# Performance work log

Measured on AMD Instinct MI355X. Metric: run time of the kernel, lower is better.

Reference implementation:

```python
import jax, jax.numpy as jnp
import numpy as np
import math

B, LQ, S, D = 8, 4096, 77, 1024
H, HD = 16, 64
R, ALPHA = 192, 16.0
LORA_SCALE = ALPHA / R
N_SUBJ = 32


def setup_inputs() -> dict:
    key = jax.random.key(0)
    ks = jax.random.split(key, 16)
    w = 0.02
    return {
        "hidden_states": jax.random.normal(ks[0], (B, LQ, D), jnp.float32),
        "encoder_hidden_states": jax.random.normal(ks[1], (B, S, D), jnp.float32),
        "Wq": jax.random.normal(ks[2], (D, D), jnp.float32) * w,
        "Wk": jax.random.normal(ks[3], (D, D), jnp.float32) * w,
        "Wv": jax.random.normal(ks[4], (D, D), jnp.float32) * w,
        "Wo": jax.random.normal(ks[5], (D, D), jnp.float32) * w,
        "bo": jnp.zeros((D,), jnp.float32),
        "Ak": jax.random.normal(ks[6], (R, D), jnp.float32) * w,
        "Bk": jax.random.normal(ks[7], (D, R), jnp.float32) * w,
        "Av": jax.random.normal(ks[8], (R, D), jnp.float32) * w,
        "Bv": jax.random.normal(ks[9], (D, R), jnp.float32) * w,
        "Ao": jax.random.normal(ks[10], (R, D), jnp.float32) * w,
        "Bo": jax.random.normal(ks[11], (D, R), jnp.float32) * w,
        "cross_attn_scale_factor": jnp.ones((), jnp.float32),
        "subj_b": jax.random.randint(ks[12], (N_SUBJ,), 0, B, jnp.int32),
        "subj_n": jax.random.randint(ks[13], (N_SUBJ,), 0, S, jnp.int32),
    }


def _lora(x, A, Bm):
    # peft LoRA delta: scale * (x @ A^T) @ B^T
    return LORA_SCALE * ((x @ A.T) @ Bm.T)


def reference(hidden_states, encoder_hidden_states, Wq, Wk, Wv, Wo, bo,
              Ak, Bk, Av, Bv, Ao, Bo, cross_attn_scale_factor, subj_b, subj_n):
    hs, ehs = hidden_states, encoder_hidden_states
    # q_lora_updates_query=False -> query uses the base projection only
    q = hs @ Wq.T                                  # [B, LQ, D]
    k = ehs @ Wk.T + _lora(ehs, Ak, Bk)            # [B, S, D] (to_k_lora)
    v = ehs @ Wv.T + _lora(ehs, Av, Bv)            # [B, S, D] (to_v_lora)

    q = q.reshape(B, LQ, H, HD).transpose(0, 2, 1, 3)   # [B,H,LQ,HD]
    k = k.reshape(B, S, H, HD).transpose(0, 2, 1, 3)    # [B,H,S,HD]
    v = v.reshape(B, S, H, HD).transpose(0, 2, 1, 3)

    scale = 1.0 / math.sqrt(HD)
    attn_score = jnp.einsum('bhld,bhsd->bhls', q, k) * scale  # [B,H,LQ,S]

    # normalize_cross_attn: zero-center subject-token scores over query dim,
    # then rescale by the learned cross_attn_scale_factor.
    sub = attn_score[subj_b, :, :, subj_n]                    # [K,H,LQ]
    sub = (sub - sub.mean(axis=2, keepdims=True)) * cross_attn_scale_factor
    attn_score = attn_score.at[subj_b, :, :, subj_n].set(sub)

    attn_weight = jax.nn.softmax(attn_score, axis=-1)
    out = jnp.einsum('bhls,bhsd->bhld', attn_weight, v)       # [B,H,LQ,HD]
    out = out.transpose(0, 2, 1, 3).reshape(B, LQ, D)

    # to_out_lora: base out-proj (with bias) + LoRA delta; to_out[1] dropout = id
    out = out @ Wo.T + bo + _lora(out, Ao, Bo)
    return out
```

## Files before the change

kernel.cpp:

```cpp
#include <hip/hip_runtime.h>
#include <stdint.h>

#define B_     8
#define LQ_    4096
#define S_     77
#define SP_    80
#define D_     1024
#define H_     16
#define HD_    64
#define NC_    1280
#define NSUBJ_ 32

typedef __attribute__((ext_vector_type(4))) float  f4;
typedef __attribute__((ext_vector_type(8))) short  short8;
typedef __attribute__((ext_vector_type(8))) unsigned short us8;
typedef __attribute__((ext_vector_type(4))) unsigned short us4;

__device__ __forceinline__ unsigned short f2bf(float f) {
  union { float f; unsigned u; } x; x.f = f;
  unsigned r = x.u + 0x7FFFu + ((x.u >> 16) & 1u);
  return (unsigned short)(r >> 16);
}

__device__ __forceinline__ void gload16(const void* g, void* s) {
  __builtin_amdgcn_global_load_lds((const __attribute__((address_space(1))) void*)g,
                                   (__attribute__((address_space(3))) void*)s, 16, 0, 0);
}

__global__ __launch_bounds__(256) void k_hssum(const float* __restrict__ hs,
                                               float* __restrict__ part,
                                               unsigned short* __restrict__ hsb) {
  int b = blockIdx.y;
  size_t base = ((size_t)b * LQ_ + (size_t)blockIdx.x * 64) * D_ + threadIdx.x * 4;
  f4 acc = {0.f, 0.f, 0.f, 0.f};
  for (int l = 0; l < 64; ++l) {
    f4 v = *(const f4*)(hs + base + (size_t)l * D_);
    acc += v;
    if (hsb) {
      us4 o;
#pragma unroll
      for (int j = 0; j < 4; ++j) o[j] = f2bf(v[j]);
      *(us4*)(hsb + base + (size_t)l * D_) = o;
    }
  }
  *(f4*)(part + (size_t)blockIdx.x * (B_ * D_) + b * D_ + threadIdx.x * 4) = acc;
}

__global__ __launch_bounds__(256) void k_hsred(const float* __restrict__ part,
                                               float* __restrict__ hssum) {
  int i = blockIdx.x * 256 + threadIdx.x;
  float s = 0.f;
  for (int x = 0; x < 64; ++x) s += part[(size_t)x * (B_ * D_) + i];
  hssum[i] = s;
}

__global__ __launch_bounds__(256) void k_tr4(const float* __restrict__ Wq, const float* __restrict__ Ak,
                                             const float* __restrict__ Av, const float* __restrict__ Ao,
                                             float* __restrict__ wqT, float* __restrict__ akT,
                                             float* __restrict__ avT, float* __restrict__ aoT) {
  int z = blockIdx.z;
  const float* in = z == 0 ? Wq : (z == 1 ? Ak : (z == 2 ? Av : Ao));
  float* out = z == 0 ? wqT : (z == 1 ? akT : (z == 2 ? avT : aoT));
  int R = z == 0 ? 1024 : 192;
  const int C = 1024;
  int c0 = blockIdx.x * 32, r0 = blockIdx.y * 32;
  if (r0 >= R) return;
  __shared__ float tile[32][33];
  int tx = threadIdx.x & 31, ty = threadIdx.x >> 5;
#pragma unroll
  for (int k = 0; k < 4; ++k)
    tile[ty + 8 * k][tx] = in[(size_t)(r0 + ty + 8 * k) * C + c0 + tx];
  __syncthreads();
#pragma unroll
  for (int k = 0; k < 4; ++k)
    out[(size_t)(c0 + ty + 8 * k) * R + r0 + tx] = tile[tx][ty + 8 * k];
}

template <bool OBF>
__device__ __forceinline__ void gemm64_body(
    const float* __restrict__ A, int lda, const float* __restrict__ Bt, int ldb,
    void* __restrict__ Cv, int ldc, long cbase, const float* __restrict__ Dm, int ldd,
    int M, int Mv, int N, int K, float alpha, int m0, int n0,
    short* As, short* Bs) {
  int t = threadIdx.x, lane = t & 63, wid = t >> 6;
  int wm = wid >> 1, wn = wid & 1;
  f4 acc[2][2] = {};
  int srow = t >> 2, skc = (t & 3) * 8;
  for (int k0 = 0; k0 < K; k0 += 32) {
    __syncthreads();
    f4 a0 = {0,0,0,0}, a1 = {0,0,0,0}, b0 = {0,0,0,0}, b1 = {0,0,0,0};
    if (m0 + srow < Mv) {
      const float* p = A + (size_t)(m0 + srow) * lda + k0 + skc;
      a0 = *(const f4*)p; a1 = *(const f4*)(p + 4);
    }
    if (n0 + srow < N) {
      const float* p = Bt + (size_t)(n0 + srow) * ldb + k0 + skc;
      b0 = *(const f4*)p; b1 = *(const f4*)(p + 4);
    }
    us8 ua, ub;
#pragma unroll
    for (int j = 0; j < 4; ++j) {
      ua[j] = f2bf(a0[j]); ua[4 + j] = f2bf(a1[j]);
      ub[j] = f2bf(b0[j]); ub[4 + j] = f2bf(b1[j]);
    }
    *(us8*)(As + srow * 40 + skc) = ua;
    *(us8*)(Bs + srow * 40 + skc) = ub;
    __syncthreads();
    short8 fa[2], fb[2];
#pragma unroll
    for (int i = 0; i < 2; ++i) {
      fa[i] = *(const short8*)(As + (wm * 32 + i * 16 + (lane & 15)) * 40 + (lane >> 4) * 8);
      fb[i] = *(const short8*)(Bs + (wn * 32 + i * 16 + (lane & 15)) * 40 + (lane >> 4) * 8);
    }
#pragma unroll
    for (int mi = 0; mi < 2; ++mi)
#pragma unroll
      for (int ni = 0; ni < 2; ++ni)
        acc[mi][ni] = __builtin_amdgcn_mfma_f32_16x16x32_bf16(fa[mi], fb[ni], acc[mi][ni], 0, 0, 0);
  }
#pragma unroll
  for (int mi = 0; mi < 2; ++mi)
#pragma unroll
    for (int ni = 0; ni < 2; ++ni)
#pragma unroll
      for (int j = 0; j < 4; ++j) {
        int row = m0 + wm * 32 + mi * 16 + (lane >> 4) * 4 + j;
        int col = n0 + wn * 32 + ni * 16 + (lane & 15);
        if (row < M && col < N) {
          float val = acc[mi][ni][j] * alpha;
          if (Dm) val += Dm[(size_t)row * ldd + col];
          size_t idx = (size_t)cbase + (size_t)row * ldc + col;
          if (OBF) ((unsigned short*)Cv)[idx] = f2bf(val);
          else     ((float*)Cv)[idx] = val;
        }
      }
}

template <bool OBF>
__global__ __launch_bounds__(256) void k_gemm_small(
    const float* __restrict__ A, int lda, long sA1, long sA2,
    const float* __restrict__ Bt, int ldb, long sB1, long sB2,
    void* __restrict__ Cv, int ldc, long sC1, long sC2,
    const float* __restrict__ Dm, int ldd,
    int M, int Mv, int N, int K, float alpha, int Z2) {
  int z = blockIdx.z, z1 = z / Z2, z2 = z - z1 * Z2;
  __shared__ short As[64 * 40];
  __shared__ short Bs[64 * 40];
  gemm64_body<OBF>(A + z1 * sA1 + z2 * sA2, lda, Bt + z1 * sB1 + z2 * sB2, ldb,
                   Cv, ldc, z1 * sC1 + z2 * sC2, Dm, ldd, M, Mv, N, K, alpha,
                   blockIdx.x * 64, blockIdx.y * 64, As, Bs);
}

__global__ __launch_bounds__(256) void k_weff(
    const float* __restrict__ Bk, const float* __restrict__ Bv, const float* __restrict__ Bo,
    const float* __restrict__ akT, const float* __restrict__ avT, const float* __restrict__ aoT,
    const float* __restrict__ Wk, const float* __restrict__ Wv, const float* __restrict__ Wo,
    float* __restrict__ weff, float alpha) {
  int z = blockIdx.z;
  const float* A  = z == 0 ? Bk : (z == 1 ? Bv : Bo);
  const float* Bt = z == 0 ? akT : (z == 1 ? avT : aoT);
  const float* Dm = z == 0 ? Wk : (z == 1 ? Wv : Wo);
  __shared__ short As[64 * 40];
  __shared__ short Bs[64 * 40];
  gemm64_body<false>(A, 192, Bt, 192, weff + (size_t)z * 1048576, 1024, 0, Dm, 1024,
                     1024, 1024, 1024, 192, alpha, blockIdx.x * 64, blockIdx.y * 64, As, Bs);
}

__global__ void k_mubeta(const float* __restrict__ hssum, const float* __restrict__ Wq,
                         const float* __restrict__ kv,
                         const int* __restrict__ sb, const int* __restrict__ sn,
                         const float* __restrict__ csf_p,
                         float* __restrict__ alphav, float* __restrict__ betav) {
  int h = blockIdx.x, b = blockIdx.y;
  int t = threadIdx.x;
  __shared__ float qp[64];
  {
    int hd = t >> 1, half = t & 1;
    const float* wr = Wq + (size_t)(h * 64 + hd) * D_ + half * 512;
    const float* hp = hssum + b * D_ + half * 512;
    float s = 0.f;
    for (int d = 0; d < 512; d += 4) {
      f4 w = *(const f4*)(wr + d);
      f4 x = *(const f4*)(hp + d);
      s += w[0] * x[0] + w[1] * x[1] + w[2] * x[2] + w[3] * x[3];
    }
    s += __shfl_xor(s, 1, 64);
    if (half == 0) qp[hd] = s * (1.f / 4096.f);
  }
  __syncthreads();
  int s = t;
  if (s >= SP_) return;
  const float* kp = kv + ((size_t)(b * SP_ + s)) * 2048 + h * HD_;
  float mu = 0.f;
#pragma unroll 8
  for (int hd = 0; hd < HD_; ++hd) mu += qp[hd] * kp[hd];
  mu *= 0.125f;
  bool subj = false;
  for (int i = 0; i < NSUBJ_; ++i) subj = subj || (sb[i] == b && sn[i] == s);
  float csf = *csf_p;
  int c = b * NC_ + h * SP_ + s;
  alphav[c] = subj ? csf : 1.f;
  betav[c] = (s >= S_) ? -1e30f : (subj ? -mu * csf : 0.f);
}

__global__ __launch_bounds__(512, 2) void k_score_big(
    const unsigned short* __restrict__ hsb, const unsigned short* __restrict__ Mt,
    const float* __restrict__ alphav, const float* __restrict__ betav,
    unsigned short* __restrict__ P) {
  extern __shared__ short lds[];
  const int ASZ = 256 * 64;
  const int BSZ = 320 * 64;
  int id = blockIdx.x;
  int x = id & 7, idp = id >> 3;
  int nt = idp & 3;
  int pid = (idp >> 2) * 8 + x;
  int b = pid >> 4, mt = pid & 15;
  int m0 = mt * 256, n0 = nt * 320;

  const unsigned short* Ab = hsb + (size_t)b * LQ_ * D_;
  const unsigned short* Bb = Mt + (size_t)b * NC_ * D_;
  const float* alp = alphav + b * NC_;
  const float* bet = betav + b * NC_;
  unsigned short* Pb = P + (size_t)b * LQ_ * NC_;

  int t = threadIdx.x, lane = t & 63, wid = t >> 6;
  int wm = wid >> 2, wn = wid & 3;
  f4 acc[8][5] = {};

  auto STAGE = [&](int bf, int k0) {
#pragma unroll
    for (int p = 0; p < 4; ++p) {
      int cb = p * 512 + wid * 64;
      int c = cb + lane;
      int row = c >> 3, col = ((c & 7) ^ (row & 7)) * 8;
      gload16(Ab + (size_t)(m0 + row) * D_ + k0 + col, (char*)(lds + bf * ASZ) + cb * 16);
    }
#pragma unroll
    for (int p = 0; p < 5; ++p) {
      int cb = p * 512 + wid * 64;
      int c = cb + lane;
      int row = c >> 3, col = ((c & 7) ^ (row & 7)) * 8;
      gload16(Bb + (size_t)(n0 + row) * D_ + k0 + col, (char*)(lds + 2 * ASZ + bf * BSZ) + cb * 16);
    }
  };

  STAGE(0, 0);
  int c = 0;
  for (int kt = 0; kt < 16; ++kt) {
    if (kt < 15) {
      STAGE(c ^ 1, (kt + 1) * 64);
      asm volatile("s_waitcnt vmcnt(9)" ::: "memory");
    } else {
      asm volatile("s_waitcnt vmcnt(0)" ::: "memory");
    }
    __builtin_amdgcn_s_barrier();
    const short* Ar = lds + c * ASZ;
    const short* Br = lds + 2 * ASZ + c * BSZ;
    __builtin_amdgcn_s_setprio(1);
#pragma unroll
    for (int kk = 0; kk < 2; ++kk) {
      int co = ((kk * 4 + (lane >> 4)) ^ (lane & 7)) * 8;
      short8 fb[5];
#pragma unroll
      for (int ni = 0; ni < 5; ++ni)
        fb[ni] = *(const short8*)(Br + (wn * 80 + ni * 16 + (lane & 15)) * 64 + co);
#pragma unroll
      for (int mi = 0; mi < 8; ++mi) {
        short8 fa = *(const short8*)(Ar + (wm * 128 + mi * 16 + (lane & 15)) * 64 + co);
#pragma unroll
        for (int ni = 0; ni < 5; ++ni)
          acc[mi][ni] = __builtin_amdgcn_mfma_f32_16x16x32_bf16(fa, fb[ni], acc[mi][ni], 0, 0, 0);
      }
    }
    __builtin_amdgcn_s_setprio(0);
    __builtin_amdgcn_s_barrier();
    c ^= 1;
  }

  float al[5], be[5];
#pragma unroll
  for (int ni = 0; ni < 5; ++ni) {
    int cc = n0 + wn * 80 + ni * 16 + (lane & 15);
    al[ni] = alp[cc]; be[ni] = bet[cc];
  }
#pragma unroll
  for (int mi = 0; mi < 8; ++mi) {
#pragma unroll
    for (int j = 0; j < 4; ++j) {
      float v[5];
      float m = -3.0e38f;
#pragma unroll
      for (int ni = 0; ni < 5; ++ni) { v[ni] = acc[mi][ni][j] * al[ni] + be[ni]; m = fmaxf(m, v[ni]); }
#pragma unroll
      for (int off = 1; off < 16; off <<= 1) m = fmaxf(m, __shfl_xor(m, off, 64));
      float ssum = 0.f;
#pragma unroll
      for (int ni = 0; ni < 5; ++ni) { v[ni] = __expf(v[ni] - m); ssum += v[ni]; }
#pragma unroll
      for (int off = 1; off < 16; off <<= 1) ssum += __shfl_xor(ssum, off, 64);
      float inv = 1.f / ssum;
      int row = m0 + wm * 128 + mi * 16 + (lane >> 4) * 4 + j;
      size_t rb = (size_t)row * NC_ + n0 + wn * 80 + (lane & 15);
#pragma unroll
      for (int ni = 0; ni < 5; ++ni)
        Pb[rb + ni * 16] = f2bf(v[ni] * inv);
    }
  }
}

__global__ __launch_bounds__(256) void k_score_f32(
    const float* __restrict__ hs, const unsigned short* __restrict__ Mt,
    const float* __restrict__ alphav, const float* __restrict__ betav,
    unsigned short* __restrict__ P) {
  int id = blockIdx.x;
  int x = id & 7, idp = id >> 3;
  int n_t = idp & 7;
  int pid = (idp >> 3) * 8 + x;
  int b = pid >> 5, m_t = pid & 31;
  int m0 = m_t * 128, n0 = n_t * 160;
  const float* Af = hs + (size_t)b * LQ_ * D_;
  const unsigned short* Bb = Mt + (size_t)b * NC_ * D_;
  const float* alp = alphav + b * NC_;
  const float* bet = betav + b * NC_;
  unsigned short* Pb = P + (size_t)b * LQ_ * NC_;
  __shared__ short As[128 * 64];
  __shared__ short Bs[160 * 64];
  int t = threadIdx.x, lane = t & 63, wid = t >> 6;
  int wm = wid >> 1, wn = wid & 1;
  int srow = lane >> 3;
  int schunk = (lane & 7) ^ srow;
  f4 acc[4][5] = {};
  for (int k0 = 0; k0 < D_; k0 += 64) {
    __syncthreads();
    for (int i = wid; i < 20; i += 4)
      gload16(Bb + (size_t)(n0 + i * 8 + srow) * D_ + k0 + schunk * 8, (char*)Bs + i * 1024);
    int arow = t >> 3, ac = t & 7;
    int awc = ac ^ (arow & 7);
#pragma unroll
    for (int p = 0; p < 4; ++p) {
      int row = p * 32 + arow;
      const float* src = Af + (size_t)(m0 + row) * D_ + k0 + ac * 8;
      f4 v0 = *(const f4*)src;
      f4 v1 = *(const f4*)(src + 4);
      us8 u;
#pragma unroll
      for (int j = 0; j < 4; ++j) { u[j] = f2bf(v0[j]); u[4 + j] = f2bf(v1[j]); }
      *(us8*)(As + row * 64 + awc * 8) = u;
    }
    __syncthreads();
#pragma unroll
    for (int kk = 0; kk < 2; ++kk) {
      int co = ((kk * 4 + (lane >> 4)) ^ (lane & 7)) * 8;
      short8 fa[4], fb[5];
#pragma unroll
      for (int mi = 0; mi < 4; ++mi)
        fa[mi] = *(const short8*)(As + (wm * 64 + mi * 16 + (lane & 15)) * 64 + co);
#pragma unroll
      for (int ni = 0; ni < 5; ++ni)
        fb[ni] = *(const short8*)(Bs + (wn * 80 + ni * 16 + (lane & 15)) * 64 + co);
#pragma unroll
      for (int mi = 0; mi < 4; ++mi)
#pragma unroll
        for (int ni = 0; ni < 5; ++ni)
          acc[mi][ni] = __builtin_amdgcn_mfma_f32_16x16x32_bf16(fa[mi], fb[ni], acc[mi][ni], 0, 0, 0);
    }
  }
  float al[5], be[5];
#pragma unroll
  for (int ni = 0; ni < 5; ++ni) {
    int cc = n0 + wn * 80 + ni * 16 + (lane & 15);
    al[ni] = alp[cc]; be[ni] = bet[cc];
  }
#pragma unroll
  for (int mi = 0; mi < 4; ++mi) {
#pragma unroll
    for (int j = 0; j < 4; ++j) {
      float v[5];
      float m = -3.0e38f;
#pragma unroll
      for (int ni = 0; ni < 5; ++ni) { v[ni] = acc[mi][ni][j] * al[ni] + be[ni]; m = fmaxf(m, v[ni]); }
#pragma unroll
      for (int off = 1; off < 16; off <<= 1) m = fmaxf(m, __shfl_xor(m, off, 64));
      float ssum = 0.f;
#pragma unroll
      for (int ni = 0; ni < 5; ++ni) { v[ni] = __expf(v[ni] - m); ssum += v[ni]; }
#pragma unroll
      for (int off = 1; off < 16; off <<= 1) ssum += __shfl_xor(ssum, off, 64);
      float inv = 1.f / ssum;
      int row = m0 + wm * 64 + mi * 16 + (lane >> 4) * 4 + j;
      size_t rb = (size_t)row * NC_ + n0 + wn * 80 + (lane & 15);
#pragma unroll
      for (int ni = 0; ni < 5; ++ni)
        Pb[rb + ni * 16] = f2bf(v[ni] * inv);
    }
  }
}

__global__ __launch_bounds__(512, 2) void k_out_big(
    const unsigned short* __restrict__ P, const unsigned short* __restrict__ Ut,
    const float* __restrict__ bo, float* __restrict__ out) {
  extern __shared__ short lds[];
  const int ASZ = 256 * 64;
  int id = blockIdx.x;
  int x = id & 7, idp = id >> 3;
  int nt = idp & 3;
  int pid = (idp >> 2) * 8 + x;
  int b = pid >> 4, mt = pid & 15;
  int m0 = mt * 256, n0 = nt * 256;

  const unsigned short* Ab = P + (size_t)b * LQ_ * NC_;
  const unsigned short* Bb = Ut + (size_t)b * D_ * NC_;
  float* ob = out + (size_t)b * LQ_ * D_;

  int t = threadIdx.x, lane = t & 63, wid = t >> 6;
  int wm = wid >> 2, wn = wid & 3;
  f4 acc[8][4] = {};
  const int T = NC_ / 64;

  auto STAGE = [&](int bf, int k0) {
#pragma unroll
    for (int p = 0; p < 4; ++p) {
      int cb = p * 512 + wid * 64;
      int c = cb + lane;
      int row = c >> 3, col = ((c & 7) ^ (row & 7)) * 8;
      gload16(Ab + (size_t)(m0 + row) * NC_ + k0 + col, (char*)(lds + bf * ASZ) + cb * 16);
    }
#pragma unroll
    for (int p = 0; p < 4; ++p) {
      int cb = p * 512 + wid * 64;
      int c = cb + lane;
      int row = c >> 3, col = ((c & 7) ^ (row & 7)) * 8;
      gload16(Bb + (size_t)(n0 + row) * NC_ + k0 + col, (char*)(lds + 2 * ASZ + bf * ASZ) + cb * 16);
    }
  };

  STAGE(0, 0);
  int c = 0;
  for (int kt = 0; kt < T; ++kt) {
    if (kt + 1 < T) {
      STAGE(c ^ 1, (kt + 1) * 64);
      asm volatile("s_waitcnt vmcnt(8)" ::: "memory");
    } else {
      asm volatile("s_waitcnt vmcnt(0)" ::: "memory");
    }
    __builtin_amdgcn_s_barrier();
    const short* Ar = lds + c * ASZ;
    const short* Br = lds + 2 * ASZ + c * ASZ;
    __builtin_amdgcn_s_setprio(1);
#pragma unroll
    for (int kk = 0; kk < 2; ++kk) {
      int co = ((kk * 4 + (lane >> 4)) ^ (lane & 7)) * 8;
      short8 fb[4];
#pragma unroll
      for (int ni = 0; ni < 4; ++ni)
        fb[ni] = *(const short8*)(Br + (wn * 64 + ni * 16 + (lane & 15)) * 64 + co);
#pragma unroll
      for (int mi = 0; mi < 8; ++mi) {
        short8 fa = *(const short8*)(Ar + (wm * 128 + mi * 16 + (lane & 15)) * 64 + co);
#pragma unroll
        for (int ni = 0; ni < 4; ++ni)
          acc[mi][ni] = __builtin_amdgcn_mfma_f32_16x16x32_bf16(fa, fb[ni], acc[mi][ni], 0, 0, 0);
      }
    }
    __builtin_amdgcn_s_setprio(0);
    __builtin_amdgcn_s_barrier();
    c ^= 1;
  }
#pragma unroll
  for (int ni = 0; ni < 4; ++ni) {
    int col = n0 + wn * 64 + ni * 16 + (lane & 15);
    float bov = bo[col];
#pragma unroll
    for (int mi = 0; mi < 8; ++mi)
#pragma unroll
      for (int j = 0; j < 4; ++j) {
        int row = m0 + wm * 128 + mi * 16 + (lane >> 4) * 4 + j;
        ob[(size_t)row * D_ + col] = acc[mi][ni][j] + bov;
      }
  }
}

extern "C" void kernel_launch(void* const* d_in, const int* in_sizes, int n_in,
                              void* d_out, int out_size, void* d_ws, size_t ws_size,
                              hipStream_t stream) {
  const float* hs  = (const float*)d_in[0];
  const float* ehs = (const float*)d_in[1];
  const float* Wq  = (const float*)d_in[2];
  const float* Wk  = (const float*)d_in[3];
  const float* Wv  = (const float*)d_in[4];
  const float* Wo  = (const float*)d_in[5];
  const float* bo  = (const float*)d_in[6];
  const float* Ak  = (const float*)d_in[7];
  const float* Bk  = (const float*)d_in[8];
  const float* Av  = (const float*)d_in[9];
  const float* Bv  = (const float*)d_in[10];
  const float* Ao  = (const float*)d_in[11];
  const float* Bo  = (const float*)d_in[12];
  const float* csf = (const float*)d_in[13];
  const int*   sb  = (const int*)d_in[14];
  const int*   sn  = (const int*)d_in[15];
  float* out = (float*)d_out;

  hipFuncSetAttribute(reinterpret_cast<const void*>(k_score_big),
                      hipFuncAttributeMaxDynamicSharedMemorySize, 147456);
  hipFuncSetAttribute(reinterpret_cast<const void*>(k_out_big),
                      hipFuncAttributeMaxDynamicSharedMemorySize, 131072);

  char* ws = (char*)d_ws;
  unsigned short* P  = (unsigned short*)ws;
  unsigned short* Mt = (unsigned short*)(ws + 83886080);
  unsigned short* Ut = (unsigned short*)(ws + 104857600);
  const size_t NEED_HSB = 125829120ULL + 67108864ULL + 81920ULL;
  bool useHsb = ws_size >= NEED_HSB;
  unsigned short* hsb = useHsb ? (unsigned short*)(ws + 125829120) : nullptr;
  char* tail = useHsb ? (ws + 192937984) : (ws + 125829120);
  float* alphav = (float*)tail;
  float* betav  = (float*)(tail + 40960);
  float* kvbuf = (float*)(ws + 0);
  float* weff  = (float*)(ws + 5242880);
  float* wqT   = (float*)(ws + 17825792);
  float* aT    = (float*)(ws + 22020096);
  float* part  = (float*)(ws + 24379392);
  float* hssum = (float*)(ws + 26476544);

  float* woE = weff + 2097152;
  float* akT = aT;
  float* avT = aT + 196608;
  float* aoT = aT + 393216;

  const float LS = 16.0f / 192.0f;

  k_hssum<<<dim3(64, 8), 256, 0, stream>>>(hs, part, hsb);
  k_hsred<<<32, 256, 0, stream>>>(part, hssum);

  k_tr4<<<dim3(32, 32, 4), 256, 0, stream>>>(Wq, Ak, Av, Ao, wqT, akT, avT, aoT);

  k_weff<<<dim3(16, 16, 3), 256, 0, stream>>>(Bk, Bv, Bo, akT, avT, aoT, Wk, Wv, Wo, weff, LS);

  k_gemm_small<false><<<dim3(2, 32, 8), 256, 0, stream>>>(
      ehs, 1024, 77L * 1024, 0, weff, 1024, 0, 0, kvbuf, 2048, 80L * 2048, 0, nullptr, 0,
      80, 77, 2048, 1024, 1.f, 1);

  k_gemm_small<true><<<dim3(2, 16, 128), 256, 0, stream>>>(
      kvbuf, 2048, 80L * 2048, 64L, wqT, 1024, 0, 64L,
      Mt, 1024, (long)NC_ * 1024, 80L * 1024, nullptr, 0,
      80, 80, 1024, 64, 0.125f, 16);

  k_gemm_small<true><<<dim3(16, 2, 128), 256, 0, stream>>>(
      woE, 1024, 0, 64L, kvbuf + 1024, 2048, 80L * 2048, 64L,
      Ut, NC_, 1024L * NC_, 80L, nullptr, 0,
      1024, 1024, 80, 64, 1.f, 16);

  k_mubeta<<<dim3(16, 8), 128, 0, stream>>>(hssum, Wq, kvbuf, sb, sn, csf, alphav, betav);

  if (useHsb)
    k_score_big<<<512, 512, 147456, stream>>>(hsb, Mt, alphav, betav, P);
  else
    k_score_f32<<<2048, 256, 0, stream>>>(hs, Mt, alphav, betav, P);
  k_out_big<<<512, 512, 131072, stream>>>(P, Ut, bo, out);

  (void)in_sizes; (void)n_in; (void)out_size; (void)ws_size;
}
```

Measured before the change: 374.2 us.

## Split GEMM k-tile into four MFMA phases with interleaved prefetch

Restructures the main loops of the score GEMM and the output GEMM into four barrier-separated phases per k-tile. Each phase issues LDS fragment loads and 20 or 16 MFMAs. The global-to-LDS prefetch of the next tile is split, with A loaded before the first phase and B loaded between phases, so memory traffic spreads across compute instead of arriving as one burst. This ping-pong style schedule adds extra barriers and relies on the vmcnt waits staying correct for the reordered loads.

```diff
diff --git a/kernel.cpp b/kernel.cpp
--- a/kernel.cpp
+++ b/kernel.cpp
@@ -225,56 +225,96 @@
 
   int t = threadIdx.x, lane = t & 63, wid = t >> 6;
   int wm = wid >> 2, wn = wid & 3;
+  int r = lane & 15, q = lane >> 4;
   f4 acc[8][5] = {};
 
-  auto STAGE = [&](int bf, int k0) {
-#pragma unroll
-    for (int p = 0; p < 4; ++p) {
-      int cb = p * 512 + wid * 64;
-      int c = cb + lane;
-      int row = c >> 3, col = ((c & 7) ^ (row & 7)) * 8;
-      gload16(Ab + (size_t)(m0 + row) * D_ + k0 + col, (char*)(lds + bf * ASZ) + cb * 16);
-    }
-#pragma unroll
-    for (int p = 0; p < 5; ++p) {
-      int cb = p * 512 + wid * 64;
-      int c = cb + lane;
-      int row = c >> 3, col = ((c & 7) ^ (row & 7)) * 8;
-      gload16(Bb + (size_t)(n0 + row) * D_ + k0 + col, (char*)(lds + 2 * ASZ + bf * BSZ) + cb * 16);
-    }
+  auto SA = [&](int bf, int k0, int p) {
+    int cb = p * 512 + wid * 64;
+    int cc = cb + lane;
+    int row = cc >> 3, col = ((cc & 7) ^ (row & 7)) * 8;
+    gload16(Ab + (size_t)(m0 + row) * D_ + k0 + col, (char*)(lds + bf * ASZ) + cb * 16);
   };
-
-  STAGE(0, 0);
-  int c = 0;
+  auto SB = [&](int bf, int k0, int p) {
+    int cb = p * 512 + wid * 64;
+    int cc = cb + lane;
+    int row = cc >> 3, col = ((cc & 7) ^ (row & 7)) * 8;
+    gload16(Bb + (size_t)(n0 + row) * D_ + k0 + col, (char*)(lds + 2 * ASZ + bf * BSZ) + cb * 16);
+  };
+
+#pragma unroll
+  for (int p = 0; p < 4; ++p) SA(0, 0, p);
+#pragma unroll
+  for (int p = 0; p < 5; ++p) SB(0, 0, p);
+
   for (int kt = 0; kt < 16; ++kt) {
-    if (kt < 15) {
-      STAGE(c ^ 1, (kt + 1) * 64);
-      asm volatile("s_waitcnt vmcnt(9)" ::: "memory");
+    int cur = kt & 1;
+    const short* Ar = lds + cur * ASZ;
+    const short* Br = lds + 2 * ASZ + cur * BSZ;
+    int k1 = (kt + 1) * 64;
+    bool pre = kt < 15;
+    int co0 = (q ^ (lane & 7)) * 8;
+    int co1 = ((4 + q) ^ (lane & 7)) * 8;
+    short8 fb[5], fa[4];
+
+    if (pre) {
+      SA(cur ^ 1, k1, 0); SA(cur ^ 1, k1, 1); SA(cur ^ 1, k1, 2); SA(cur ^ 1, k1, 3);
+      SB(cur ^ 1, k1, 0);
+      asm volatile("s_waitcnt vmcnt(5)" ::: "memory");
     } else {
       asm volatile("s_waitcnt vmcnt(0)" ::: "memory");
     }
     __builtin_amdgcn_s_barrier();
-    const short* Ar = lds + c * ASZ;
-    const short* Br = lds + 2 * ASZ + c * BSZ;
-    __builtin_amdgcn_s_setprio(1);
-#pragma unroll
-    for (int kk = 0; kk < 2; ++kk) {
-      int co = ((kk * 4 + (lane >> 4)) ^ (lane & 7)) * 8;
-      short8 fb[5];
+#pragma unroll
+    for (int ni = 0; ni < 5; ++ni) fb[ni] = *(const short8*)(Br + (wn * 80 + ni * 16 + r) * 64 + co0);
+#pragma unroll
+    for (int mi = 0; mi < 4; ++mi) fa[mi] = *(const short8*)(Ar + (wm * 128 + mi * 16 + r) * 64 + co0);
+    __builtin_amdgcn_s_setprio(1);
+#pragma unroll
+    for (int mi = 0; mi < 4; ++mi)
 #pragma unroll
       for (int ni = 0; ni < 5; ++ni)
-        fb[ni] = *(const short8*)(Br + (wn * 80 + ni * 16 + (lane & 15)) * 64 + co);
-#pragma unroll
-      for (int mi = 0; mi < 8; ++mi) {
-        short8 fa = *(const short8*)(Ar + (wm * 128 + mi * 16 + (lane & 15)) * 64 + co);
-#pragma unroll
-        for (int ni = 0; ni < 5; ++ni)
-          acc[mi][ni] = __builtin_amdgcn_mfma_f32_16x16x32_bf16(fa, fb[ni], acc[mi][ni], 0, 0, 0);
-      }
-    }
-    __builtin_amdgcn_s_setprio(0);
-    __builtin_amdgcn_s_barrier();
-    c ^= 1;
+        acc[mi][ni] = __builtin_amdgcn_mfma_f32_16x16x32_bf16(fa[mi], fb[ni], acc[mi][ni], 0, 0, 0);
+    __builtin_amdgcn_s_setprio(0);
+    __builtin_amdgcn_s_barrier();
+
+#pragma unroll
+    for (int mi = 0; mi < 4; ++mi) fa[mi] = *(const short8*)(Ar + (wm * 128 + (4 + mi) * 16 + r) * 64 + co0);
+    if (pre) { SB(cur ^ 1, k1, 1); SB(cur ^ 1, k1, 2); SB(cur ^ 1, k1, 3); SB(cur ^ 1, k1, 4); }
+    __builtin_amdgcn_s_barrier();
+    __builtin_amdgcn_s_setprio(1);
+#pragma unroll
+    for (int mi = 0; mi < 4; ++mi)
+#pragma unroll
+      for (int ni = 0; ni < 5; ++ni)
+        acc[4 + mi][ni] = __builtin_amdgcn_mfma_f32_16x16x32_bf16(fa[mi], fb[ni], acc[4 + mi][ni], 0, 0, 0);
+    __builtin_amdgcn_s_setprio(0);
+    __builtin_amdgcn_s_barrier();
+
+#pragma unroll
+    for (int ni = 0; ni < 5; ++ni) fb[ni] = *(const short8*)(Br + (wn * 80 + ni * 16 + r) * 64 + co1);
+#pragma unroll
+    for (int mi = 0; mi < 4; ++mi) fa[mi] = *(const short8*)(Ar + (wm * 128 + mi * 16 + r) * 64 + co1);
+    __builtin_amdgcn_s_barrier();
+    __builtin_amdgcn_s_setprio(1);
+#pragma unroll
+    for (int mi = 0; mi < 4; ++mi)
+#pragma unroll
+      for (int ni = 0; ni < 5; ++ni)
+        acc[mi][ni] = __builtin_amdgcn_mfma_f32_16x16x32_bf16(fa[mi], fb[ni], acc[mi][ni], 0, 0, 0);
+    __builtin_amdgcn_s_setprio(0);
+    __builtin_amdgcn_s_barrier();
+
+#pragma unroll
+    for (int mi = 0; mi < 4; ++mi) fa[mi] = *(const short8*)(Ar + (wm * 128 + (4 + mi) * 16 + r) * 64 + co1);
+    __builtin_amdgcn_s_barrier();
+    __builtin_amdgcn_s_setprio(1);
+#pragma unroll
+    for (int mi = 0; mi < 4; ++mi)
+#pragma unroll
+      for (int ni = 0; ni < 5; ++ni)
+        acc[4 + mi][ni] = __builtin_amdgcn_mfma_f32_16x16x32_bf16(fa[mi], fb[ni], acc[4 + mi][ni], 0, 0, 0);
+    __builtin_amdgcn_s_setprio(0);
+    __builtin_amdgcn_s_barrier();
   }
 
   float al[5], be[5];
@@ -414,58 +454,98 @@
 
   int t = threadIdx.x, lane = t & 63, wid = t >> 6;
   int wm = wid >> 2, wn = wid & 3;
+  int r = lane & 15, q = lane >> 4;
   f4 acc[8][4] = {};
   const int T = NC_ / 64;
 
-  auto STAGE = [&](int bf, int k0) {
-#pragma unroll
-    for (int p = 0; p < 4; ++p) {
-      int cb = p * 512 + wid * 64;
-      int c = cb + lane;
-      int row = c >> 3, col = ((c & 7) ^ (row & 7)) * 8;
-      gload16(Ab + (size_t)(m0 + row) * NC_ + k0 + col, (char*)(lds + bf * ASZ) + cb * 16);
-    }
-#pragma unroll
-    for (int p = 0; p < 4; ++p) {
-      int cb = p * 512 + wid * 64;
-      int c = cb + lane;
-      int row = c >> 3, col = ((c & 7) ^ (row & 7)) * 8;
-      gload16(Bb + (size_t)(n0 + row) * NC_ + k0 + col, (char*)(lds + 2 * ASZ + bf * ASZ) + cb * 16);
-    }
+  auto SA = [&](int bf, int k0, int p) {
+    int cb = p * 512 + wid * 64;
+    int cc = cb + lane;
+    int row = cc >> 3, col = ((cc & 7) ^ (row & 7)) * 8;
+    gload16(Ab + (size_t)(m0 + row) * NC_ + k0 + col, (char*)(lds + bf * ASZ) + cb * 16);
   };
-
-  STAGE(0, 0);
-  int c = 0;
+  auto SB = [&](int bf, int k0, int p) {
+    int cb = p * 512 + wid * 64;
+    int cc = cb + lane;
+    int row = cc >> 3, col = ((cc & 7) ^ (row & 7)) * 8;
+    gload16(Bb + (size_t)(n0 + row) * NC_ + k0 + col, (char*)(lds + 2 * ASZ + bf * ASZ) + cb * 16);
+  };
+
+#pragma unroll
+  for (int p = 0; p < 4; ++p) SA(0, 0, p);
+#pragma unroll
+  for (int p = 0; p < 4; ++p) SB(0, 0, p);
+
   for (int kt = 0; kt < T; ++kt) {
-    if (kt + 1 < T) {
-      STAGE(c ^ 1, (kt + 1) * 64);
-      asm volatile("s_waitcnt vmcnt(8)" ::: "memory");
+    int cur = kt & 1;
+    const short* Ar = lds + cur * ASZ;
+    const short* Br = lds + 2 * ASZ + cur * ASZ;
+    int k1 = (kt + 1) * 64;
+    bool pre = kt + 1 < T;
+    int co0 = (q ^ (lane & 7)) * 8;
+    int co1 = ((4 + q) ^ (lane & 7)) * 8;
+    short8 fb[4], fa[4];
+
+    if (pre) {
+      SA(cur ^ 1, k1, 0); SA(cur ^ 1, k1, 1); SA(cur ^ 1, k1, 2); SA(cur ^ 1, k1, 3);
+      asm volatile("s_waitcnt vmcnt(4)" ::: "memory");
     } else {
       asm volatile("s_waitcnt vmcnt(0)" ::: "memory");
     }
     __builtin_amdgcn_s_barrier();
-    const short* Ar = lds + c * ASZ;
-    const short* Br = lds + 2 * ASZ + c * ASZ;
-    __builtin_amdgcn_s_setprio(1);
-#pragma unroll
-    for (int kk = 0; kk < 2; ++kk) {
-      int co = ((kk * 4 + (lane >> 4)) ^ (lane & 7)) * 8;
-      short8 fb[4];
+#pragma unroll
+    for (int ni = 0; ni < 4; ++ni) fb[ni] = *(const short8*)(Br + (wn * 64 + ni * 16 + r) * 64 + co0);
+#pragma unroll
+    for (int mi = 0; mi < 4; ++mi) fa[mi] = *(const short8*)(Ar + (wm * 128 + mi * 16 + r) * 64 + co0);
+    __builtin_amdgcn_s_setprio(1);
+#pragma unroll
+    for (int mi = 0; mi < 4; ++mi)
 #pragma unroll
       for (int ni = 0; ni < 4; ++ni)
-        fb[ni] = *(const short8*)(Br + (wn * 64 + ni * 16 + (lane & 15)) * 64 + co);
-#pragma unroll
-      for (int mi = 0; mi < 8; ++mi) {
-        short8 fa = *(const short8*)(Ar + (wm * 128 + mi * 16 + (lane & 15)) * 64 + co);
-#pragma unroll
-        for (int ni = 0; ni < 4; ++ni)
-          acc[mi][ni] = __builtin_amdgcn_mfma_f32_16x16x32_bf16(fa, fb[ni], acc[mi][ni], 0, 0, 0);
-      }
-    }
-    __builtin_amdgcn_s_setprio(0);
-    __builtin_amdgcn_s_barrier();
-    c ^= 1;
-  }
+        acc[mi][ni] = __builtin_amdgcn_mfma_f32_16x16x32_bf16(fa[mi], fb[ni], acc[mi][ni], 0, 0, 0);
+    __builtin_amdgcn_s_setprio(0);
+    __builtin_amdgcn_s_barrier();
+
+#pragma unroll
+    for (int mi = 0; mi < 4; ++mi) fa[mi] = *(const short8*)(Ar + (wm * 128 + (4 + mi) * 16 + r) * 64 + co0);
+    if (pre) { SB(cur ^ 1, k1, 0); SB(cur ^ 1, k1, 1); SB(cur ^ 1, k1, 2); SB(cur ^ 1, k1, 3); }
+    __builtin_amdgcn_s_barrier();
+    __builtin_amdgcn_s_setprio(1);
+#pragma unroll
+    for (int mi = 0; mi < 4; ++mi)
+#pragma unroll
+      for (int ni = 0; ni < 4; ++ni)
+        acc[4 + mi][ni] = __builtin_amdgcn_mfma_f32_16x16x32_bf16(fa[mi], fb[ni], acc[4 + mi][ni], 0, 0, 0);
+    __builtin_amdgcn_s_setprio(0);
+    __builtin_amdgcn_s_barrier();
+
+#pragma unroll
+    for (int ni = 0; ni < 4; ++ni) fb[ni] = *(const short8*)(Br + (wn * 64 + ni * 16 + r) * 64 + co1);
+#pragma unroll
+    for (int mi = 0; mi < 4; ++mi) fa[mi] = *(const short8*)(Ar + (wm * 128 + mi * 16 + r) * 64 + co1);
+    __builtin_amdgcn_s_barrier();
+    __builtin_amdgcn_s_setprio(1);
+#pragma unroll
+    for (int mi = 0; mi < 4; ++mi)
+#pragma unroll
+      for (int ni = 0; ni < 4; ++ni)
+        acc[mi][ni] = __builtin_amdgcn_mfma_f32_16x16x32_bf16(fa[mi], fb[ni], acc[mi][ni], 0, 0, 0);
+    __builtin_amdgcn_s_setprio(0);
+    __builtin_amdgcn_s_barrier();
+
+#pragma unroll
+    for (int mi = 0; mi < 4; ++mi) fa[mi] = *(const short8*)(Ar + (wm * 128 + (4 + mi) * 16 + r) * 64 + co1);
+    __builtin_amdgcn_s_barrier();
+    __builtin_amdgcn_s_setprio(1);
+#pragma unroll
+    for (int mi = 0; mi < 4; ++mi)
+#pragma unroll
+      for (int ni = 0; ni < 4; ++ni)
+        acc[4 + mi][ni] = __builtin_amdgcn_mfma_f32_16x16x32_bf16(fa[mi], fb[ni], acc[4 + mi][ni], 0, 0, 0);
+    __builtin_amdgcn_s_setprio(0);
+    __builtin_amdgcn_s_barrier();
+  }
+
 #pragma unroll
   for (int ni = 0; ni < 4; ++ni) {
     int col = n0 + wn * 64 + ni * 16 + (lane & 15);
```

New measurement: 364.6 us. -2.6%, faster.

## Shrink GEMM tiles and K-step to raise occupancy in score and output kernels

Applied to the files above, without the earlier changes.

Both big GEMM kernels move from 256x320/256x256 tiles with K-step 64 to 256x160/256x128 tiles with K-step 32. Waves are laid out 4x2, the LDS swizzle is redone for 32-wide rows, and launch bounds go to 4 blocks per CU with twice as many blocks. The aim is to cut LDS footprint and register pressure so more waves stay resident and can hide latency. In exchange there is less reuse per tile, more global traffic for the shared operand, and twice as many barriers per K.

```diff
diff --git a/kernel.cpp b/kernel.cpp
--- a/kernel.cpp
+++ b/kernel.cpp
@@ -203,19 +203,19 @@
   betav[c] = (s >= S_) ? -1e30f : (subj ? -mu * csf : 0.f);
 }
 
-__global__ __launch_bounds__(512, 2) void k_score_big(
+__global__ __launch_bounds__(512, 4) void k_score_big(
     const unsigned short* __restrict__ hsb, const unsigned short* __restrict__ Mt,
     const float* __restrict__ alphav, const float* __restrict__ betav,
     unsigned short* __restrict__ P) {
   extern __shared__ short lds[];
-  const int ASZ = 256 * 64;
-  const int BSZ = 320 * 64;
+  short* A0 = lds;
+  short* B0 = lds + 16384;
   int id = blockIdx.x;
   int x = id & 7, idp = id >> 3;
-  int nt = idp & 3;
-  int pid = (idp >> 2) * 8 + x;
+  int nt = idp & 7;
+  int pid = (idp >> 3) * 8 + x;
   int b = pid >> 4, mt = pid & 15;
-  int m0 = mt * 256, n0 = nt * 320;
+  int m0 = mt * 256, n0 = nt * 160;
 
   const unsigned short* Ab = hsb + (size_t)b * LQ_ * D_;
   const unsigned short* Bb = Mt + (size_t)b * NC_ * D_;
@@ -224,67 +224,71 @@
   unsigned short* Pb = P + (size_t)b * LQ_ * NC_;
 
   int t = threadIdx.x, lane = t & 63, wid = t >> 6;
-  int wm = wid >> 2, wn = wid & 3;
-  f4 acc[8][5] = {};
-
+  int wm = wid >> 1, wn = wid & 1;
+  int r = lane & 15, q = lane >> 4;
+  f4 acc[4][5] = {};
+
+  auto SA = [&](int bf, int k0, int p) {
+    int cb = p * 512 + wid * 64;
+    int cc = cb + lane;
+    int row = cc >> 2, gc = (cc & 3) ^ ((row >> 1) & 3);
+    gload16(Ab + (size_t)(m0 + row) * D_ + k0 + gc * 8, (char*)(A0 + bf * 8192) + cb * 16);
+  };
+  auto SB = [&](int bf, int k0, int p) {
+    int cb = p * 512 + wid * 64;
+    int cc = cb + lane;
+    int row = cc >> 2, gc = (cc & 3) ^ ((row >> 1) & 3);
+    gload16(Bb + (size_t)(n0 + row) * D_ + k0 + gc * 8, (char*)(B0 + bf * 5120) + cb * 16);
+  };
   auto STAGE = [&](int bf, int k0) {
-#pragma unroll
-    for (int p = 0; p < 4; ++p) {
-      int cb = p * 512 + wid * 64;
-      int c = cb + lane;
-      int row = c >> 3, col = ((c & 7) ^ (row & 7)) * 8;
-      gload16(Ab + (size_t)(m0 + row) * D_ + k0 + col, (char*)(lds + bf * ASZ) + cb * 16);
-    }
-#pragma unroll
-    for (int p = 0; p < 5; ++p) {
-      int cb = p * 512 + wid * 64;
-      int c = cb + lane;
-      int row = c >> 3, col = ((c & 7) ^ (row & 7)) * 8;
-      gload16(Bb + (size_t)(n0 + row) * D_ + k0 + col, (char*)(lds + 2 * ASZ + bf * BSZ) + cb * 16);
-    }
+    SA(bf, k0, 0); SA(bf, k0, 1);
+    SB(bf, k0, 0);
+    if (wid < 2) SB(bf, k0, 1);
   };
 
   STAGE(0, 0);
-  int c = 0;
-  for (int kt = 0; kt < 16; ++kt) {
-    if (kt < 15) {
-      STAGE(c ^ 1, (kt + 1) * 64);
-      asm volatile("s_waitcnt vmcnt(9)" ::: "memory");
+  int cur = 0;
+  for (int kt = 0; kt < 32; ++kt) {
+    if (kt < 31) {
+      STAGE(cur ^ 1, (kt + 1) * 32);
+      if (wid < 2) asm volatile("s_waitcnt vmcnt(4)" ::: "memory");
+      else         asm volatile("s_waitcnt vmcnt(3)" ::: "memory");
     } else {
       asm volatile("s_waitcnt vmcnt(0)" ::: "memory");
     }
     __builtin_amdgcn_s_barrier();
-    const short* Ar = lds + c * ASZ;
-    const short* Br = lds + 2 * ASZ + c * BSZ;
+    const short* Ar = A0 + cur * 8192;
+    const short* Br = B0 + cur * 5120;
+    short8 fa[4], fb[5];
+#pragma unroll
+    for (int ni = 0; ni < 5; ++ni) {
+      int row = wn * 80 + ni * 16 + r;
+      fb[ni] = *(const short8*)(Br + row * 32 + ((q ^ ((row >> 1) & 3)) * 8));
+    }
+#pragma unroll
+    for (int mi = 0; mi < 4; ++mi) {
+      int row = wm * 64 + mi * 16 + r;
+      fa[mi] = *(const short8*)(Ar + row * 32 + ((q ^ ((row >> 1) & 3)) * 8));
+    }
     __builtin_amdgcn_s_setprio(1);
 #pragma unroll
-    for (int kk = 0; kk < 2; ++kk) {
-      int co = ((kk * 4 + (lane >> 4)) ^ (lane & 7)) * 8;
-      short8 fb[5];
+    for (int mi = 0; mi < 4; ++mi)
 #pragma unroll
       for (int ni = 0; ni < 5; ++ni)
-        fb[ni] = *(const short8*)(Br + (wn * 80 + ni * 16 + (lane & 15)) * 64 + co);
-#pragma unroll
-      for (int mi = 0; mi < 8; ++mi) {
-        short8 fa = *(const short8*)(Ar + (wm * 128 + mi * 16 + (lane & 15)) * 64 + co);
-#pragma unroll
-        for (int ni = 0; ni < 5; ++ni)
-          acc[mi][ni] = __builtin_amdgcn_mfma_f32_16x16x32_bf16(fa, fb[ni], acc[mi][ni], 0, 0, 0);
-      }
-    }
+        acc[mi][ni] = __builtin_amdgcn_mfma_f32_16x16x32_bf16(fa[mi], fb[ni], acc[mi][ni], 0, 0, 0);
     __builtin_amdgcn_s_setprio(0);
     __builtin_amdgcn_s_barrier();
-    c ^= 1;
+    cur ^= 1;
   }
 
   float al[5], be[5];
 #pragma unroll
   for (int ni = 0; ni < 5; ++ni) {
-    int cc = n0 + wn * 80 + ni * 16 + (lane & 15);
+    int cc = n0 + wn * 80 + ni * 16 + r;
     al[ni] = alp[cc]; be[ni] = bet[cc];
   }
 #pragma unroll
-  for (int mi = 0; mi < 8; ++mi) {
+  for (int mi = 0; mi < 4; ++mi) {
 #pragma unroll
     for (int j = 0; j < 4; ++j) {
       float v[5];
@@ -299,8 +303,8 @@
 #pragma unroll
       for (int off = 1; off < 16; off <<= 1) ssum += __shfl_xor(ssum, off, 64);
       float inv = 1.f / ssum;
-      int row = m0 + wm * 128 + mi * 16 + (lane >> 4) * 4 + j;
-      size_t rb = (size_t)row * NC_ + n0 + wn * 80 + (lane & 15);
+      int row = m0 + wm * 64 + mi * 16 + q * 4 + j;
+      size_t rb = (size_t)row * NC_ + n0 + wn * 80 + r;
 #pragma unroll
       for (int ni = 0; ni < 5; ++ni)
         Pb[rb + ni * 16] = f2bf(v[ni] * inv);
@@ -396,85 +400,86 @@
   }
 }
 
-__global__ __launch_bounds__(512, 2) void k_out_big(
+__global__ __launch_bounds__(512, 4) void k_out_big(
     const unsigned short* __restrict__ P, const unsigned short* __restrict__ Ut,
     const float* __restrict__ bo, float* __restrict__ out) {
   extern __shared__ short lds[];
-  const int ASZ = 256 * 64;
+  short* A0 = lds;
+  short* B0 = lds + 16384;
   int id = blockIdx.x;
   int x = id & 7, idp = id >> 3;
-  int nt = idp & 3;
-  int pid = (idp >> 2) * 8 + x;
+  int nt = idp & 7;
+  int pid = (idp >> 3) * 8 + x;
   int b = pid >> 4, mt = pid & 15;
-  int m0 = mt * 256, n0 = nt * 256;
+  int m0 = mt * 256, n0 = nt * 128;
 
   const unsigned short* Ab = P + (size_t)b * LQ_ * NC_;
   const unsigned short* Bb = Ut + (size_t)b * D_ * NC_;
   float* ob = out + (size_t)b * LQ_ * D_;
 
   int t = threadIdx.x, lane = t & 63, wid = t >> 6;
-  int wm = wid >> 2, wn = wid & 3;
-  f4 acc[8][4] = {};
-  const int T = NC_ / 64;
-
-  auto STAGE = [&](int bf, int k0) {
-#pragma unroll
-    for (int p = 0; p < 4; ++p) {
-      int cb = p * 512 + wid * 64;
-      int c = cb + lane;
-      int row = c >> 3, col = ((c & 7) ^ (row & 7)) * 8;
-      gload16(Ab + (size_t)(m0 + row) * NC_ + k0 + col, (char*)(lds + bf * ASZ) + cb * 16);
-    }
-#pragma unroll
-    for (int p = 0; p < 4; ++p) {
-      int cb = p * 512 + wid * 64;
-      int c = cb + lane;
-      int row = c >> 3, col = ((c & 7) ^ (row & 7)) * 8;
-      gload16(Bb + (size_t)(n0 + row) * NC_ + k0 + col, (char*)(lds + 2 * ASZ + bf * ASZ) + cb * 16);
-    }
+  int wm = wid >> 1, wn = wid & 1;
+  int r = lane & 15, q = lane >> 4;
+  f4 acc[4][4] = {};
+  const int T = NC_ / 32;
+
+  auto SA = [&](int bf, int k0, int p) {
+    int cb = p * 512 + wid * 64;
+    int cc = cb + lane;
+    int row = cc >> 2, gc = (cc & 3) ^ ((row >> 1) & 3);
+    gload16(Ab + (size_t)(m0 + row) * NC_ + k0 + gc * 8, (char*)(A0 + bf * 8192) + cb * 16);
   };
+  auto SB = [&](int bf, int k0) {
+    int cb = wid * 64;
+    int cc = cb + lane;
+    int row = cc >> 2, gc = (cc & 3) ^ ((row >> 1) & 3);
+    gload16(Bb + (size_t)(n0 + row) * NC_ + k0 + gc * 8, (char*)(B0 + bf * 4096) + cb * 16);
+  };
+  auto STAGE = [&](int bf, int k0) { SA(bf, k0, 0); SA(bf, k0, 1); SB(bf, k0); };
 
   STAGE(0, 0);
-  int c = 0;
+  int cur = 0;
   for (int kt = 0; kt < T; ++kt) {
     if (kt + 1 < T) {
-      STAGE(c ^ 1, (kt + 1) * 64);
-      asm volatile("s_waitcnt vmcnt(8)" ::: "memory");
+      STAGE(cur ^ 1, (kt + 1) * 32);
+      asm volatile("s_waitcnt vmcnt(3)" ::: "memory");
     } else {
       asm volatile("s_waitcnt vmcnt(0)" ::: "memory");
     }
     __builtin_amdgcn_s_barrier();
-    const short* Ar = lds + c * ASZ;
-    const short* Br = lds + 2 * ASZ + c * ASZ;
+    const short* Ar = A0 + cur * 8192;
+    const short* Br = B0 + cur * 4096;
+    short8 fa[4], fb[4];
+#pragma unroll
+    for (int ni = 0; ni < 4; ++ni) {
+      int row = wn * 64 + ni * 16 + r;
+      fb[ni] = *(const short8*)(Br + row * 32 + ((q ^ ((row >> 1) & 3)) * 8));
+    }
+#pragma unroll
+    for (int mi = 0; mi < 4; ++mi) {
+      int row = wm * 64 + mi * 16 + r;
+      fa[mi] = *(const short8*)(Ar + row * 32 + ((q ^ ((row >> 1) & 3)) * 8));
+    }
     __builtin_amdgcn_s_setprio(1);
 #pragma unroll
-    for (int kk = 0; kk < 2; ++kk) {
-      int co = ((kk * 4 + (lane >> 4)) ^ (lane & 7)) * 8;
-      short8 fb[4];
+    for (int mi = 0; mi < 4; ++mi)
 #pragma unroll
       for (int ni = 0; ni < 4; ++ni)
-        fb[ni] = *(const short8*)(Br + (wn * 64 + ni * 16 + (lane & 15)) * 64 + co);
-#pragma unroll
-      for (int mi = 0; mi < 8; ++mi) {
-        short8 fa = *(const short8*)(Ar + (wm * 128 + mi * 16 + (lane & 15)) * 64 + co);
-#pragma unroll
-        for (int ni = 0; ni < 4; ++ni)
-          acc[mi][ni] = __builtin_amdgcn_mfma_f32_16x16x32_bf16(fa, fb[ni], acc[mi][ni], 0, 0, 0);
-      }
-    }
+        acc[mi][ni] = __builtin_amdgcn_mfma_f32_16x16x32_bf16(fa[mi], fb[ni], acc[mi][ni], 0, 0, 0);
     __builtin_amdgcn_s_setprio(0);
     __builtin_amdgcn_s_barrier();
-    c ^= 1;
-  }
+    cur ^= 1;
+  }
+
 #pragma unroll
   for (int ni = 0; ni < 4; ++ni) {
-    int col = n0 + wn * 64 + ni * 16 + (lane & 15);
+    int col = n0 + wn * 64 + ni * 16 + r;
     float bov = bo[col];
 #pragma unroll
-    for (int mi = 0; mi < 8; ++mi)
+    for (int mi = 0; mi < 4; ++mi)
 #pragma unroll
       for (int j = 0; j < 4; ++j) {
-        int row = m0 + wm * 128 + mi * 16 + (lane >> 4) * 4 + j;
+        int row = m0 + wm * 64 + mi * 16 + q * 4 + j;
         ob[(size_t)row * D_ + col] = acc[mi][ni][j] + bov;
       }
   }
@@ -502,9 +507,9 @@
   float* out = (float*)d_out;
 
   hipFuncSetAttribute(reinterpret_cast<const void*>(k_score_big),
-                      hipFuncAttributeMaxDynamicSharedMemorySize, 147456);
+                      hipFuncAttributeMaxDynamicSharedMemorySize, 53248);
   hipFuncSetAttribute(reinterpret_cast<const void*>(k_out_big),
-                      hipFuncAttributeMaxDynamicSharedMemorySize, 131072);
+                      hipFuncAttributeMaxDynamicSharedMemorySize, 49152);
 
   char* ws = (char*)d_ws;
   unsigned short* P  = (unsigned short*)ws;
@@ -554,10 +559,10 @@
   k_mubeta<<<dim3(16, 8), 128, 0, stream>>>(hssum, Wq, kvbuf, sb, sn, csf, alphav, betav);
 
   if (useHsb)
-    k_score_big<<<512, 512, 147456, stream>>>(hsb, Mt, alphav, betav, P);
+    k_score_big<<<1024, 512, 53248, stream>>>(hsb, Mt, alphav, betav, P);
   else
     k_score_f32<<<2048, 256, 0, stream>>>(hs, Mt, alphav, betav, P);
-  k_out_big<<<512, 512, 131072, stream>>>(P, Ut, bo, out);
+  k_out_big<<<1024, 512, 49152, stream>>>(P, Ut, bo, out);
 
   (void)in_sizes; (void)n_in; (void)out_size; (void)ws_size;
 }
```

After: 383.4 us. 1.02x slower.
